# Kernel tuning notes

Hardware: AMD Instinct MI355X
Metric: run time of the kernel (lower is better)

The kernel has to match this reference:

```python
import jax, jax.numpy as jnp
import numpy as np

CONFIDENCE = 0.1
EPS = 1e-3  # keras BatchNormalization default epsilon
B, H, W, C = 4, 64, 64, 256


def setup_inputs() -> dict:
    key = jax.random.key(0)
    ks = jax.random.split(key, 6)
    return {
        "x": jax.random.normal(ks[0], (B, H, W, C), jnp.float32),
        "ca_gamma": jnp.ones((C,), jnp.float32),
        "ca_beta": jnp.zeros((C,), jnp.float32),
        "ca_mean": jnp.zeros((C,), jnp.float32),
        "ca_var": jnp.ones((C,), jnp.float32),
        "wq": jax.random.normal(ks[1], (C, C), jnp.float32) * 0.05,
        "wk": jax.random.normal(ks[2], (C, C), jnp.float32) * 0.05,
        "wv": jax.random.normal(ks[3], (C, C), jnp.float32) * 0.05,
        "wp": jax.random.normal(ks[4], (C, C), jnp.float32) * 0.05,
        "bn_gamma": jnp.ones((C,), jnp.float32),
        "bn_beta": jnp.zeros((C,), jnp.float32),
        "bn_mean": jnp.zeros((C,), jnp.float32),
        "bn_var": jnp.ones((C,), jnp.float32),
        "w_qkv": jax.random.normal(ks[5], (C, 3), jnp.float32) * 0.05,
    }


def _bn(x, g, b, m, v):
    # keras BatchNormalization, inference mode
    return (x - m) * jax.lax.rsqrt(v + EPS) * g + b


def reference(x, ca_gamma, ca_beta, ca_mean, ca_var, wq, wk, wv, wp,
              bn_gamma, bn_beta, bn_mean, bn_var, w_qkv):
    b, h, w, c = x.shape
    # ---- ChannelAttention (TRACER Channel_Tracer; dropout = identity at inference) ----
    gap = x.mean(axis=(1, 2))                         # [B, C] global average pool
    gn = _bn(gap, ca_gamma, ca_beta, ca_mean, ca_var)  # [B, C]
    q = gn @ wq                                        # 1x1 conv on 1x1 map == matmul
    k = gn @ wk
    v = gn @ wv
    logits = q[:, :, None] * k[:, None, :]             # [B, C, C], head_dim = 1
    score = jax.nn.softmax(logits, axis=-1)
    att = jnp.einsum('bij,bj->bi', score, v)           # [B, C]
    cmask = jax.nn.sigmoid(att @ wp)                   # [B, C] channel mask (alpha)
    ca_out = x * cmask[:, None, None, :] + x           # residual channel re-weighting
    # ---- UnionAttention spatial part ----
    co = _bn(ca_out, bn_gamma, bn_beta, bn_mean, bn_var)
    thr = jnp.percentile(cmask, CONFIDENCE * 100.0, axis=-1,
                         keepdims=True, method='linear')  # [B, 1]
    pmask = jnp.where(cmask > thr, cmask, 0.0)          # percentile masking
    co = co * pmask[:, None, None, :]
    qkv = jnp.einsum('bhwc,cf->bhwf', co, w_qkv)        # [B, H, W, 3] fused q/k/v 1x1 conv
    n = h * w
    qs = qkv[..., 0].reshape(b, n)                      # [B, N], head_dim = 1
    ks_ = qkv[..., 1].reshape(b, n)
    vs = qkv[..., 2].reshape(b, n)
    sl = qs[:, :, None] * ks_[:, None, :]               # [B, N, N] scores (outer product)
    sw = jax.nn.softmax(sl, axis=-1)
    sa = jnp.einsum('bij,bj->bi', sw, vs)               # [B, N]
    return qkv[..., 2:3] + sa.reshape(b, h, w, 1)       # v + attention, [B, H, W, 1]
```

## Files before the change

kernel.cpp:

```cpp
#include <hip/hip_runtime.h>

#define EPS 1e-3f

#define OFF_PGAP   0
#define OFF_PART   65536
#define OFF_AW     163840
#define OFF_BIAS   164864
#define OFF_QS     164880
#define OFF_KS     181264
#define OFF_VS     197648

__global__ __launch_bounds__(512) void k_gap(
    const float* __restrict__ x,
    const float* __restrict__ wq, const float* __restrict__ wk,
    const float* __restrict__ wv, const float* __restrict__ wp,
    const float* __restrict__ bng, const float* __restrict__ bnb,
    const float* __restrict__ bnm, const float* __restrict__ bnv,
    const float* __restrict__ cag, const float* __restrict__ cab,
    const float* __restrict__ cam, const float* __restrict__ cav,
    float* __restrict__ pgap)
{
    __shared__ float4 s4[512];
    int blk = blockIdx.x;
    int t = threadIdx.x;
    int lane = t & 63, sub = t >> 6;

    if (t < 256) {
        const float* wmat = (blk < 64) ? wq : (blk < 128) ? wk
                          : (blk < 192) ? wv : wp;
        float4 w4 = *(const float4*)(wmat + (size_t)(blk & 63) * 1024 + 4 * t);
        asm volatile("" :: "v"(w4.x), "v"(w4.y), "v"(w4.z), "v"(w4.w));
    }
    if (blk == 1 && t < 256) {
        float z = bng[t] + bnb[t] + bnm[t] + bnv[t];
        asm volatile("" :: "v"(z));
    }
    if (blk == 2 && t < 256) {
        float z = cag[t] + cab[t] + cam[t] + cav[t];
        asm volatile("" :: "v"(z));
    }

    const float* xp = x + ((size_t)blk * 64 + sub * 8) * 256 + 4 * lane;
    float4 s = make_float4(0.f, 0.f, 0.f, 0.f);
    #pragma unroll
    for (int u = 0; u < 8; ++u) {
        float4 v = *(const float4*)(xp + (size_t)u * 256);
        s.x += v.x; s.y += v.y; s.z += v.z; s.w += v.w;
    }
    s4[sub * 64 + lane] = s;
    __syncthreads();
    if (t < 64) {
        float4 o = s4[t];
        #pragma unroll
        for (int p = 1; p < 8; ++p) {
            float4 v = s4[p * 64 + t];
            o.x += v.x; o.y += v.y; o.z += v.z; o.w += v.w;
        }
        *(float4*)(pgap + blk * 256 + 4 * t) = o;
    }
}

__global__ __launch_bounds__(512) void k_qkvmat(
    const float* __restrict__ pgap,
    const float* __restrict__ cag, const float* __restrict__ cab,
    const float* __restrict__ cam, const float* __restrict__ cav,
    const float* __restrict__ wq, const float* __restrict__ wk,
    const float* __restrict__ wv,
    float* __restrict__ part)
{
    __shared__ float gpart[512];
    __shared__ float gn_s[32];
    __shared__ float red[2048];
    int blk = blockIdx.x;
    int m = blk / 32, g = blk % 32;
    int r0 = g * 8;
    int t = threadIdx.x;
    const float* W = (m == 0) ? wq : (m == 1) ? wk : wv;

    {
        int b = t >> 7, row = (t >> 4) & 7, p4 = t & 15;
        float s = 0.f;
        #pragma unroll
        for (int q = 0; q < 4; ++q)
            s += pgap[(size_t)(b * 64 + p4 * 4 + q) * 256 + r0 + row];
        gpart[b * 128 + row * 16 + p4] = s;
    }
    __syncthreads();
    if (t < 32) {
        int b = t >> 3, row = t & 7;
        float s = 0.f;
        #pragma unroll
        for (int p = 0; p < 16; ++p) s += gpart[b * 128 + row * 16 + p];
        float gv = s * (1.0f / 4096.0f);
        int c = r0 + row;
        float sc = cag[c] * rsqrtf(cav[c] + EPS);
        gn_s[b * 8 + row] = gv * sc + (cab[c] - cam[c] * sc);
    }
    __syncthreads();
    {
        int c = t & 255, h = t >> 8;
        float a0 = 0.f, a1 = 0.f, a2 = 0.f, a3 = 0.f;
        #pragma unroll
        for (int rr = 0; rr < 4; ++rr) {
            int ri = h * 4 + rr;
            float w = W[(size_t)(r0 + ri) * 256 + c];
            a0 = fmaf(gn_s[0 * 8 + ri], w, a0);
            a1 = fmaf(gn_s[1 * 8 + ri], w, a1);
            a2 = fmaf(gn_s[2 * 8 + ri], w, a2);
            a3 = fmaf(gn_s[3 * 8 + ri], w, a3);
        }
        red[(h * 4 + 0) * 256 + c] = a0;
        red[(h * 4 + 1) * 256 + c] = a1;
        red[(h * 4 + 2) * 256 + c] = a2;
        red[(h * 4 + 3) * 256 + c] = a3;
    }
    __syncthreads();
    {
        int b = t >> 7, c0 = (t & 127) * 2;
        float v0 = red[b * 256 + c0]     + red[(4 + b) * 256 + c0];
        float v1 = red[b * 256 + c0 + 1] + red[(4 + b) * 256 + c0 + 1];
        *(float2*)(part + (size_t)((m * 32 + g) * 4 + b) * 256 + c0) =
            make_float2(v0, v1);
    }
}

__global__ __launch_bounds__(512) void k_mid(
    const float* __restrict__ part, const float* __restrict__ wp,
    const float* __restrict__ bng, const float* __restrict__ bnb,
    const float* __restrict__ bnm, const float* __restrict__ bnv,
    const float* __restrict__ wqkv,
    float* __restrict__ Aw, float* __restrict__ biasW)
{
    __shared__ float sq[256], sk[256], sv[256], att[256], cmv[256], Bc[256];
    __shared__ float red[2048];
    __shared__ float swq[768];
    __shared__ float sc2[8];
    int b = blockIdx.x;
    int t = threadIdx.x;
    int lane = t & 63, sub = t >> 6;

    if (t < 384) { swq[t] = wqkv[t]; swq[t + 384] = wqkv[t + 384]; }

    if (t < 384) {
        int m = t >> 7, c0 = (t & 127) * 2;
        float a0 = 0.f, a1 = 0.f;
        #pragma unroll 8
        for (int g = 0; g < 32; ++g) {
            float2 v = *(const float2*)(part +
                          (size_t)((m * 32 + g) * 4 + b) * 256 + c0);
            a0 += v.x; a1 += v.y;
        }
        float* dst = (m == 0) ? sq : (m == 1) ? sk : sv;
        dst[c0] = a0; dst[c0 + 1] = a1;
    }
    __syncthreads();

    if (t < 64) {
        float mx = -1e30f, mn = 1e30f;
        #pragma unroll
        for (int u = 0; u < 4; ++u) {
            float v = sk[t + u * 64];
            mx = fmaxf(mx, v); mn = fminf(mn, v);
        }
        #pragma unroll
        for (int m2 = 1; m2 < 64; m2 <<= 1) {
            mx = fmaxf(mx, __shfl_xor(mx, m2, 64));
            mn = fminf(mn, __shfl_xor(mn, m2, 64));
        }
        if (t == 0) { sc2[0] = mx; sc2[1] = mn; }
    }
    __syncthreads();

    {
        int c = t & 255, h = t >> 8;
        float a = sq[c];
        float m = (a >= 0.f) ? a * sc2[0] : a * sc2[1];
        const float* skp = sk + h * 128;
        const float* svp = sv + h * 128;
        float den = 0.f, num = 0.f;
        #pragma unroll 4
        for (int j = 0; j < 128; ++j) {
            float e = __expf(fmaf(a, skp[j], -m));
            den += e; num = fmaf(e, svp[j], num);
        }
        red[h * 256 + c] = den;
        red[512 + h * 256 + c] = num;
    }
    __syncthreads();
    if (t < 256)
        att[t] = (red[512 + t] + red[768 + t]) / (red[t] + red[256 + t]);
    __syncthreads();

    {
        int rg = sub, c4 = lane * 4;
        float4 ac = make_float4(0.f, 0.f, 0.f, 0.f);
        const float* wpp = wp + (size_t)rg * 32 * 256 + c4;
        #pragma unroll 8
        for (int i = 0; i < 32; ++i) {
            float g = att[rg * 32 + i];
            float4 w = *(const float4*)(wpp + (size_t)i * 256);
            ac.x = fmaf(g, w.x, ac.x); ac.y = fmaf(g, w.y, ac.y);
            ac.z = fmaf(g, w.z, ac.z); ac.w = fmaf(g, w.w, ac.w);
        }
        *(float4*)(red + rg * 256 + c4) = ac;
    }
    __syncthreads();
    if (t < 256) {
        float ac = 0.f;
        #pragma unroll
        for (int r = 0; r < 8; ++r) ac += red[r * 256 + t];
        cmv[t] = 1.0f / (1.0f + __expf(-ac));
    }
    __syncthreads();

    if (t < 256) {
        float my = cmv[t];
        int rank = 0;
        for (int j = 0; j < 256; ++j) {
            float o = cmv[j];
            rank += (o < my) ? 1 : ((o == my && j < t) ? 1 : 0);
        }
        if (rank == 25) sc2[2] = my;
        if (rank == 26) sc2[3] = my;
    }
    __syncthreads();
    if (t == 0) sc2[4] = sc2[2] + 0.5f * (sc2[3] - sc2[2]);
    __syncthreads();

    if (t < 256) {
        float s2 = bng[t] * rsqrtf(bnv[t] + EPS);
        float o2 = bnb[t] - bnm[t] * s2;
        float cc = cmv[t];
        float pm = (cc > sc2[4]) ? cc : 0.f;
        Aw[b * 256 + t] = (1.f + cc) * s2 * pm;
        Bc[t] = o2 * pm;
    }
    __syncthreads();
    if (t < 3) {
        float s3 = 0.f;
        for (int ch = 0; ch < 256; ++ch)
            s3 = fmaf(Bc[ch], swq[ch * 3 + t], s3);
        biasW[b * 3 + t] = s3;
    }
}

__global__ __launch_bounds__(256) void k_qkv(
    const float* __restrict__ x, const float* __restrict__ A,
    const float* __restrict__ wqkv, const float* __restrict__ bias,
    float* __restrict__ qs, float* __restrict__ ks, float* __restrict__ vs)
{
    int lane = threadIdx.x & 63;
    int wid = (blockIdx.x * 256 + threadIdx.x) >> 6;
    float4 wA = *(const float4*)(wqkv + 12 * lane);
    float4 wB = *(const float4*)(wqkv + 12 * lane + 4);
    float4 wC = *(const float4*)(wqkv + 12 * lane + 8);
    float w00 = wA.x, w01 = wA.y, w02 = wA.z;
    float w10 = wA.w, w11 = wB.x, w12 = wB.y;
    float w20 = wB.z, w21 = wB.w, w22 = wC.x;
    float w30 = wC.y, w31 = wC.z, w32 = wC.w;
    #pragma unroll
    for (int b = 0; b < 4; ++b) {
        int pix = b * 4096 + wid;
        float4 xv = *(const float4*)(x + (size_t)pix * 256 + 4 * lane);
        float4 A4 = *(const float4*)(A + b * 256 + 4 * lane);
        float t0 = xv.x * A4.x, t1 = xv.y * A4.y;
        float t2 = xv.z * A4.z, t3 = xv.w * A4.w;
        float q = t0 * w00 + t1 * w10 + t2 * w20 + t3 * w30;
        float k = t0 * w01 + t1 * w11 + t2 * w21 + t3 * w31;
        float v = t0 * w02 + t1 * w12 + t2 * w22 + t3 * w32;
        #pragma unroll
        for (int m = 1; m < 64; m <<= 1) {
            q += __shfl_xor(q, m, 64);
            k += __shfl_xor(k, m, 64);
            v += __shfl_xor(v, m, 64);
        }
        if (lane == 0) {
            qs[pix] = q + bias[b * 3 + 0];
            ks[pix] = k + bias[b * 3 + 1];
            vs[pix] = v + bias[b * 3 + 2];
        }
    }
}

__global__ __launch_bounds__(512) void k_attn2(
    const float* __restrict__ qs, const float* __restrict__ ks,
    const float* __restrict__ vs, float* __restrict__ out)
{
    __shared__ float4 skv[2048];
    __shared__ float pden[8][64], pnum[8][64];
    __shared__ float rmax[8], rmin[8];
    int blk = blockIdx.x;
    int b = blk >> 6, ic = blk & 63;
    int t = threadIdx.x;
    int lane = t & 63, sub = t >> 6;
    int base = b * 4096;

    const float4* k4 = (const float4*)(ks + base);
    const float4* v4 = (const float4*)(vs + base);
    float kmx = -1e30f, kmn = 1e30f;
    #pragma unroll
    for (int u = 0; u < 2; ++u) {
        int i = t + u * 512;
        float4 kk = k4[i], vv = v4[i];
        skv[i * 2]     = make_float4(kk.x, vv.x, kk.y, vv.y);
        skv[i * 2 + 1] = make_float4(kk.z, vv.z, kk.w, vv.w);
        kmx = fmaxf(kmx, fmaxf(fmaxf(kk.x, kk.y), fmaxf(kk.z, kk.w)));
        kmn = fminf(kmn, fminf(fminf(kk.x, kk.y), fminf(kk.z, kk.w)));
    }
    #pragma unroll
    for (int m2 = 1; m2 < 64; m2 <<= 1) {
        kmx = fmaxf(kmx, __shfl_xor(kmx, m2, 64));
        kmn = fminf(kmn, __shfl_xor(kmn, m2, 64));
    }
    if (lane == 0) { rmax[sub] = kmx; rmin[sub] = kmn; }
    __syncthreads();
    float mx = rmax[0], mn = rmin[0];
    #pragma unroll
    for (int s = 1; s < 8; ++s) { mx = fmaxf(mx, rmax[s]); mn = fminf(mn, rmin[s]); }

    int row = ic * 64 + lane;
    float a = qs[base + row];
    float m = (a >= 0.f) ? a * mx : a * mn;
    float den0 = 0.f, num0 = 0.f, den1 = 0.f, num1 = 0.f;
    const float4* sp = skv + sub * 256;
    #pragma unroll 4
    for (int j = 0; j < 256; ++j) {
        float4 kv = sp[j];
        float e0 = __expf(fmaf(a, kv.x, -m));
        float e1 = __expf(fmaf(a, kv.z, -m));
        den0 += e0; num0 = fmaf(e0, kv.y, num0);
        den1 += e1; num1 = fmaf(e1, kv.w, num1);
    }
    pden[sub][lane] = den0 + den1;
    pnum[sub][lane] = num0 + num1;
    __syncthreads();
    if (t < 64) {
        float den = 0.f, num = 0.f;
        #pragma unroll
        for (int s = 0; s < 8; ++s) { den += pden[s][t]; num += pnum[s][t]; }
        int r = ic * 64 + t;
        float vrow = (r & 1) ? skv[r >> 1].w : skv[r >> 1].y;
        out[base + r] = vrow + num / den;
    }
}

extern "C" void kernel_launch(void* const* d_in, const int* in_sizes, int n_in,
                              void* d_out, int out_size, void* d_ws, size_t ws_size,
                              hipStream_t stream) {
    const float* x    = (const float*)d_in[0];
    const float* cag  = (const float*)d_in[1];
    const float* cab  = (const float*)d_in[2];
    const float* cam  = (const float*)d_in[3];
    const float* cav  = (const float*)d_in[4];
    const float* wq   = (const float*)d_in[5];
    const float* wk   = (const float*)d_in[6];
    const float* wv   = (const float*)d_in[7];
    const float* wp   = (const float*)d_in[8];
    const float* bng  = (const float*)d_in[9];
    const float* bnb  = (const float*)d_in[10];
    const float* bnm  = (const float*)d_in[11];
    const float* bnv  = (const float*)d_in[12];
    const float* wqkv = (const float*)d_in[13];

    float* ws   = (float*)d_ws;
    float* pgap = ws + OFF_PGAP;
    float* part = ws + OFF_PART;
    float* Aw   = ws + OFF_AW;
    float* bias = ws + OFF_BIAS;
    float* qs   = ws + OFF_QS;
    float* ks   = ws + OFF_KS;
    float* vs   = ws + OFF_VS;

    k_gap<<<dim3(256), dim3(512), 0, stream>>>(x, wq, wk, wv, wp,
                                               bng, bnb, bnm, bnv,
                                               cag, cab, cam, cav, pgap);
    k_qkvmat<<<dim3(96), dim3(512), 0, stream>>>(pgap, cag, cab, cam, cav,
                                                 wq, wk, wv, part);
    k_mid<<<dim3(4), dim3(512), 0, stream>>>(part, wp, bng, bnb, bnm, bnv,
                                             wqkv, Aw, bias);
    k_qkv<<<dim3(1024), dim3(256), 0, stream>>>(x, Aw, wqkv, bias, qs, ks, vs);
    k_attn2<<<dim3(256), dim3(512), 0, stream>>>(qs, ks, vs, (float*)d_out);
}
```

Before: 130.5 us.

## Fuse qkv matmul and mid stage via last-block atomic counter; widen qkv projection

Merges k_qkvmat and k_mid into one kernel: every block writes its partial products with agent-scope stores, increments a global counter, and the last four blocks of each generation wait on the counter and then run the per-batch softmax, percentile and mask stage. This removes one kernel launch and the gap between launches. k_qkv now has each wave handle two pixels with 8 channels per lane, halving the grid and the shuffle depth. Both softmax loops switch to exp2 with log2(e) pre-scaling. The spin-wait relies on all 96 blocks being co-resident and on a persistent modulo-96 counter, which carries deadlock and ordering risk.

```diff
diff --git a/kernel.cpp b/kernel.cpp
--- a/kernel.cpp
+++ b/kernel.cpp
@@ -3,12 +3,22 @@
 #define EPS 1e-3f
 
 #define OFF_PGAP   0
-#define OFF_PART   65536
-#define OFF_AW     163840
-#define OFF_BIAS   164864
-#define OFF_QS     164880
-#define OFF_KS     181264
-#define OFF_VS     197648
+#define OFF_PART   81920
+#define OFF_AW     196608
+#define OFF_BIAS   198656
+#define OFF_QS     215040
+#define OFF_KS     231424
+#define OFF_VS     247808
+
+#define L2E 1.4426950408889634f
+
+__device__ __forceinline__ void st_wt2(float* p, float a, float b) {
+    union { float f[2]; unsigned long long u; } x; x.f[0] = a; x.f[1] = b;
+    __hip_atomic_store((unsigned long long*)p, x.u, __ATOMIC_RELAXED,
+                       __HIP_MEMORY_SCOPE_AGENT);
+}
+
+__device__ unsigned g_done;
 
 __global__ __launch_bounds__(512) void k_gap(
     const float* __restrict__ x,
@@ -60,187 +70,211 @@
     }
 }
 
-__global__ __launch_bounds__(512) void k_qkvmat(
+__global__ __launch_bounds__(512) void k_qkvmid(
     const float* __restrict__ pgap,
     const float* __restrict__ cag, const float* __restrict__ cab,
     const float* __restrict__ cam, const float* __restrict__ cav,
     const float* __restrict__ wq, const float* __restrict__ wk,
-    const float* __restrict__ wv,
-    float* __restrict__ part)
+    const float* __restrict__ wv, const float* __restrict__ wp,
+    const float* __restrict__ bng, const float* __restrict__ bnb,
+    const float* __restrict__ bnm, const float* __restrict__ bnv,
+    const float* __restrict__ wqkv,
+    float* __restrict__ part, float* __restrict__ Aw, float* __restrict__ biasW)
 {
-    __shared__ float gpart[512];
-    __shared__ float gn_s[32];
-    __shared__ float red[2048];
+    __shared__ float smem[4360];
+    __shared__ int sBatch;
     int blk = blockIdx.x;
     int m = blk / 32, g = blk % 32;
     int r0 = g * 8;
     int t = threadIdx.x;
+    int lane = t & 63, sub = t >> 6;
     const float* W = (m == 0) ? wq : (m == 1) ? wk : wv;
 
     {
-        int b = t >> 7, row = (t >> 4) & 7, p4 = t & 15;
-        float s = 0.f;
-        #pragma unroll
-        for (int q = 0; q < 4; ++q)
-            s += pgap[(size_t)(b * 64 + p4 * 4 + q) * 256 + r0 + row];
-        gpart[b * 128 + row * 16 + p4] = s;
+        float* gpart = smem;
+        float* gn_s  = smem + 512;
+        float* red   = smem + 1536;
+        {
+            int b = t >> 7, row = (t >> 4) & 7, p4 = t & 15;
+            float s = 0.f;
+            #pragma unroll
+            for (int q = 0; q < 4; ++q)
+                s += pgap[(size_t)(b * 64 + p4 * 4 + q) * 256 + r0 + row];
+            gpart[b * 128 + row * 16 + p4] = s;
+        }
+        __syncthreads();
+        if (t < 32) {
+            int b = t >> 3, row = t & 7;
+            float s = 0.f;
+            #pragma unroll
+            for (int p = 0; p < 16; ++p) s += gpart[b * 128 + row * 16 + p];
+            float gv = s * (1.0f / 4096.0f);
+            int c = r0 + row;
+            float sc = cag[c] * rsqrtf(cav[c] + EPS);
+            gn_s[b * 8 + row] = gv * sc + (cab[c] - cam[c] * sc);
+        }
+        __syncthreads();
+        {
+            int c = t & 255, h = t >> 8;
+            float a0 = 0.f, a1 = 0.f, a2 = 0.f, a3 = 0.f;
+            #pragma unroll
+            for (int rr = 0; rr < 4; ++rr) {
+                int ri = h * 4 + rr;
+                float w = W[(size_t)(r0 + ri) * 256 + c];
+                a0 = fmaf(gn_s[0 * 8 + ri], w, a0);
+                a1 = fmaf(gn_s[1 * 8 + ri], w, a1);
+                a2 = fmaf(gn_s[2 * 8 + ri], w, a2);
+                a3 = fmaf(gn_s[3 * 8 + ri], w, a3);
+            }
+            red[(h * 4 + 0) * 256 + c] = a0;
+            red[(h * 4 + 1) * 256 + c] = a1;
+            red[(h * 4 + 2) * 256 + c] = a2;
+            red[(h * 4 + 3) * 256 + c] = a3;
+        }
+        __syncthreads();
+        {
+            int b = t >> 7, c0 = (t & 127) * 2;
+            float v0 = red[b * 256 + c0]     + red[(4 + b) * 256 + c0];
+            float v1 = red[b * 256 + c0 + 1] + red[(4 + b) * 256 + c0 + 1];
+            st_wt2(part + (size_t)((m * 32 + g) * 4 + b) * 256 + c0, v0, v1);
+        }
     }
     __syncthreads();
-    if (t < 32) {
-        int b = t >> 3, row = t & 7;
-        float s = 0.f;
-        #pragma unroll
-        for (int p = 0; p < 16; ++p) s += gpart[b * 128 + row * 16 + p];
-        float gv = s * (1.0f / 4096.0f);
-        int c = r0 + row;
-        float sc = cag[c] * rsqrtf(cav[c] + EPS);
-        gn_s[b * 8 + row] = gv * sc + (cab[c] - cam[c] * sc);
+    if (t == 0) {
+        unsigned v = __hip_atomic_fetch_add(&g_done, 1u, __ATOMIC_ACQ_REL,
+                                            __HIP_MEMORY_SCOPE_AGENT);
+        unsigned r = v % 96u;
+        int batch = (int)r - 92;
+        if (batch >= 0) {
+            unsigned target = v - r + 96u;
+            unsigned tries = 0;
+            while (__hip_atomic_load(&g_done, __ATOMIC_RELAXED,
+                                     __HIP_MEMORY_SCOPE_AGENT) < target) {
+                __builtin_amdgcn_s_sleep(1);
+                if (++tries > 8000000u) break;
+            }
+        }
+        sBatch = batch;
     }
     __syncthreads();
+    if (sBatch < 0) return;
+
     {
-        int c = t & 255, h = t >> 8;
-        float a0 = 0.f, a1 = 0.f, a2 = 0.f, a3 = 0.f;
-        #pragma unroll
-        for (int rr = 0; rr < 4; ++rr) {
-            int ri = h * 4 + rr;
-            float w = W[(size_t)(r0 + ri) * 256 + c];
-            a0 = fmaf(gn_s[0 * 8 + ri], w, a0);
-            a1 = fmaf(gn_s[1 * 8 + ri], w, a1);
-            a2 = fmaf(gn_s[2 * 8 + ri], w, a2);
-            a3 = fmaf(gn_s[3 * 8 + ri], w, a3);
-        }
-        red[(h * 4 + 0) * 256 + c] = a0;
-        red[(h * 4 + 1) * 256 + c] = a1;
-        red[(h * 4 + 2) * 256 + c] = a2;
-        red[(h * 4 + 3) * 256 + c] = a3;
-    }
-    __syncthreads();
-    {
-        int b = t >> 7, c0 = (t & 127) * 2;
-        float v0 = red[b * 256 + c0]     + red[(4 + b) * 256 + c0];
-        float v1 = red[b * 256 + c0 + 1] + red[(4 + b) * 256 + c0 + 1];
-        *(float2*)(part + (size_t)((m * 32 + g) * 4 + b) * 256 + c0) =
-            make_float2(v0, v1);
-    }
-}
-
-__global__ __launch_bounds__(512) void k_mid(
-    const float* __restrict__ part, const float* __restrict__ wp,
-    const float* __restrict__ bng, const float* __restrict__ bnb,
-    const float* __restrict__ bnm, const float* __restrict__ bnv,
-    const float* __restrict__ wqkv,
-    float* __restrict__ Aw, float* __restrict__ biasW)
-{
-    __shared__ float sq[256], sk[256], sv[256], att[256], cmv[256], Bc[256];
-    __shared__ float red[2048];
-    __shared__ float swq[768];
-    __shared__ float sc2[8];
-    int b = blockIdx.x;
-    int t = threadIdx.x;
-    int lane = t & 63, sub = t >> 6;
-
-    if (t < 384) { swq[t] = wqkv[t]; swq[t + 384] = wqkv[t + 384]; }
-
-    if (t < 384) {
-        int m = t >> 7, c0 = (t & 127) * 2;
-        float a0 = 0.f, a1 = 0.f;
-        #pragma unroll 8
-        for (int g = 0; g < 32; ++g) {
-            float2 v = *(const float2*)(part +
-                          (size_t)((m * 32 + g) * 4 + b) * 256 + c0);
-            a0 += v.x; a1 += v.y;
-        }
-        float* dst = (m == 0) ? sq : (m == 1) ? sk : sv;
-        dst[c0] = a0; dst[c0 + 1] = a1;
-    }
-    __syncthreads();
-
-    if (t < 64) {
-        float mx = -1e30f, mn = 1e30f;
-        #pragma unroll
-        for (int u = 0; u < 4; ++u) {
-            float v = sk[t + u * 64];
-            mx = fmaxf(mx, v); mn = fminf(mn, v);
-        }
-        #pragma unroll
-        for (int m2 = 1; m2 < 64; m2 <<= 1) {
-            mx = fmaxf(mx, __shfl_xor(mx, m2, 64));
-            mn = fminf(mn, __shfl_xor(mn, m2, 64));
-        }
-        if (t == 0) { sc2[0] = mx; sc2[1] = mn; }
-    }
-    __syncthreads();
-
-    {
-        int c = t & 255, h = t >> 8;
-        float a = sq[c];
-        float m = (a >= 0.f) ? a * sc2[0] : a * sc2[1];
-        const float* skp = sk + h * 128;
-        const float* svp = sv + h * 128;
-        float den = 0.f, num = 0.f;
-        #pragma unroll 4
-        for (int j = 0; j < 128; ++j) {
-            float e = __expf(fmaf(a, skp[j], -m));
-            den += e; num = fmaf(e, svp[j], num);
-        }
-        red[h * 256 + c] = den;
-        red[512 + h * 256 + c] = num;
-    }
-    __syncthreads();
-    if (t < 256)
-        att[t] = (red[512 + t] + red[768 + t]) / (red[t] + red[256 + t]);
-    __syncthreads();
-
-    {
-        int rg = sub, c4 = lane * 4;
-        float4 ac = make_float4(0.f, 0.f, 0.f, 0.f);
-        const float* wpp = wp + (size_t)rg * 32 * 256 + c4;
-        #pragma unroll 8
-        for (int i = 0; i < 32; ++i) {
-            float g = att[rg * 32 + i];
-            float4 w = *(const float4*)(wpp + (size_t)i * 256);
-            ac.x = fmaf(g, w.x, ac.x); ac.y = fmaf(g, w.y, ac.y);
-            ac.z = fmaf(g, w.z, ac.z); ac.w = fmaf(g, w.w, ac.w);
-        }
-        *(float4*)(red + rg * 256 + c4) = ac;
-    }
-    __syncthreads();
-    if (t < 256) {
-        float ac = 0.f;
-        #pragma unroll
-        for (int r = 0; r < 8; ++r) ac += red[r * 256 + t];
-        cmv[t] = 1.0f / (1.0f + __expf(-ac));
-    }
-    __syncthreads();
-
-    if (t < 256) {
-        float my = cmv[t];
-        int rank = 0;
-        for (int j = 0; j < 256; ++j) {
-            float o = cmv[j];
-            rank += (o < my) ? 1 : ((o == my && j < t) ? 1 : 0);
-        }
-        if (rank == 25) sc2[2] = my;
-        if (rank == 26) sc2[3] = my;
-    }
-    __syncthreads();
-    if (t == 0) sc2[4] = sc2[2] + 0.5f * (sc2[3] - sc2[2]);
-    __syncthreads();
-
-    if (t < 256) {
-        float s2 = bng[t] * rsqrtf(bnv[t] + EPS);
-        float o2 = bnb[t] - bnm[t] * s2;
-        float cc = cmv[t];
-        float pm = (cc > sc2[4]) ? cc : 0.f;
-        Aw[b * 256 + t] = (1.f + cc) * s2 * pm;
-        Bc[t] = o2 * pm;
-    }
-    __syncthreads();
-    if (t < 3) {
-        float s3 = 0.f;
-        for (int ch = 0; ch < 256; ++ch)
-            s3 = fmaf(Bc[ch], swq[ch * 3 + t], s3);
-        biasW[b * 3 + t] = s3;
+        int b = sBatch;
+        float* sq  = smem;
+        float* sk  = smem + 256;
+        float* sv  = smem + 512;
+        float* att = smem + 768;
+        float* cmv = smem + 1024;
+        float* Bc  = smem + 1280;
+        float* red = smem + 1536;
+        float* swq = smem + 3584;
+        float* sc2 = smem + 4352;
+
+        if (t < 384) { swq[t] = wqkv[t]; swq[t + 384] = wqkv[t + 384]; }
+
+        if (t < 384) {
+            int mm = t >> 7, c0 = (t & 127) * 2;
+            float a0 = 0.f, a1 = 0.f;
+            #pragma unroll 8
+            for (int gg = 0; gg < 32; ++gg) {
+                float2 v = *(const float2*)(part +
+                              (size_t)((mm * 32 + gg) * 4 + b) * 256 + c0);
+                a0 += v.x; a1 += v.y;
+            }
+            float* dst = (mm == 0) ? sq : (mm == 1) ? sk : sv;
+            dst[c0] = a0; dst[c0 + 1] = a1;
+        }
+        __syncthreads();
+
+        if (t < 64) {
+            float mx = -1e30f, mn = 1e30f;
+            #pragma unroll
+            for (int u = 0; u < 4; ++u) {
+                float v = sk[t + u * 64];
+                mx = fmaxf(mx, v); mn = fminf(mn, v);
+            }
+            #pragma unroll
+            for (int m2 = 1; m2 < 64; m2 <<= 1) {
+                mx = fmaxf(mx, __shfl_xor(mx, m2, 64));
+                mn = fminf(mn, __shfl_xor(mn, m2, 64));
+            }
+            if (t == 0) { sc2[0] = mx; sc2[1] = mn; }
+        }
+        __syncthreads();
+
+        {
+            int c = t & 255, h = t >> 8;
+            float a = sq[c];
+            float mrow = (a >= 0.f) ? a * sc2[0] : a * sc2[1];
+            float a2 = a * L2E, m2 = mrow * L2E;
+            const float* skp = sk + h * 128;
+            const float* svp = sv + h * 128;
+            float den = 0.f, num = 0.f;
+            #pragma unroll 4
+            for (int j = 0; j < 128; ++j) {
+                float e = __builtin_amdgcn_exp2f(fmaf(a2, skp[j], -m2));
+                den += e; num = fmaf(e, svp[j], num);
+            }
+            red[h * 256 + c] = den;
+            red[512 + h * 256 + c] = num;
+        }
+        __syncthreads();
+        if (t < 256)
+            att[t] = (red[512 + t] + red[768 + t]) / (red[t] + red[256 + t]);
+        __syncthreads();
+
+        {
+            int rg = sub, c4 = lane * 4;
+            float4 ac = make_float4(0.f, 0.f, 0.f, 0.f);
+            const float* wpp = wp + (size_t)rg * 32 * 256 + c4;
+            #pragma unroll 8
+            for (int i = 0; i < 32; ++i) {
+                float gv = att[rg * 32 + i];
+                float4 w = *(const float4*)(wpp + (size_t)i * 256);
+                ac.x = fmaf(gv, w.x, ac.x); ac.y = fmaf(gv, w.y, ac.y);
+                ac.z = fmaf(gv, w.z, ac.z); ac.w = fmaf(gv, w.w, ac.w);
+            }
+            *(float4*)(red + rg * 256 + c4) = ac;
+        }
+        __syncthreads();
+        if (t < 256) {
+            float ac = 0.f;
+            #pragma unroll
+            for (int r = 0; r < 8; ++r) ac += red[r * 256 + t];
+            cmv[t] = 1.0f / (1.0f + __expf(-ac));
+        }
+        __syncthreads();
+
+        if (t < 256) {
+            float my = cmv[t];
+            int rank = 0;
+            for (int j = 0; j < 256; ++j) {
+                float o = cmv[j];
+                rank += (o < my) ? 1 : ((o == my && j < t) ? 1 : 0);
+            }
+            if (rank == 25) sc2[2] = my;
+            if (rank == 26) sc2[3] = my;
+        }
+        __syncthreads();
+        if (t == 0) sc2[4] = sc2[2] + 0.5f * (sc2[3] - sc2[2]);
+        __syncthreads();
+
+        if (t < 256) {
+            float s2 = bng[t] * rsqrtf(bnv[t] + EPS);
+            float o2 = bnb[t] - bnm[t] * s2;
+            float cc = cmv[t];
+            float pm = (cc > sc2[4]) ? cc : 0.f;
+            Aw[b * 256 + t] = (1.f + cc) * s2 * pm;
+            Bc[t] = o2 * pm;
+        }
+        __syncthreads();
+        if (t < 3) {
+            float s3 = 0.f;
+            for (int ch = 0; ch < 256; ++ch)
+                s3 = fmaf(Bc[ch], swq[ch * 3 + t], s3);
+            biasW[b * 3 + t] = s3;
+        }
     }
 }
 
@@ -249,35 +283,44 @@
     const float* __restrict__ wqkv, const float* __restrict__ bias,
     float* __restrict__ qs, float* __restrict__ ks, float* __restrict__ vs)
 {
-    int lane = threadIdx.x & 63;
-    int wid = (blockIdx.x * 256 + threadIdx.x) >> 6;
-    float4 wA = *(const float4*)(wqkv + 12 * lane);
-    float4 wB = *(const float4*)(wqkv + 12 * lane + 4);
-    float4 wC = *(const float4*)(wqkv + 12 * lane + 8);
-    float w00 = wA.x, w01 = wA.y, w02 = wA.z;
-    float w10 = wA.w, w11 = wB.x, w12 = wB.y;
-    float w20 = wB.z, w21 = wB.w, w22 = wC.x;
-    float w30 = wC.y, w31 = wC.z, w32 = wC.w;
+    int t = threadIdx.x;
+    int lane = t & 63;
+    int sl = lane & 31;
+    int half = lane >> 5;
+    int wid = (blockIdx.x * 256 + t) >> 6;
+    union { float4 v4[6]; float f[24]; } W;
+    #pragma unroll
+    for (int i = 0; i < 6; ++i)
+        W.v4[i] = *(const float4*)(wqkv + 24 * sl + 4 * i);
     #pragma unroll
     for (int b = 0; b < 4; ++b) {
-        int pix = b * 4096 + wid;
-        float4 xv = *(const float4*)(x + (size_t)pix * 256 + 4 * lane);
-        float4 A4 = *(const float4*)(A + b * 256 + 4 * lane);
-        float t0 = xv.x * A4.x, t1 = xv.y * A4.y;
-        float t2 = xv.z * A4.z, t3 = xv.w * A4.w;
-        float q = t0 * w00 + t1 * w10 + t2 * w20 + t3 * w30;
-        float k = t0 * w01 + t1 * w11 + t2 * w21 + t3 * w31;
-        float v = t0 * w02 + t1 * w12 + t2 * w22 + t3 * w32;
+        int pix = b * 4096 + wid * 2 + half;
+        const float* xp = x + (size_t)pix * 256 + sl * 8;
+        float4 xv0 = *(const float4*)(xp);
+        float4 xv1 = *(const float4*)(xp + 4);
+        float4 a0 = *(const float4*)(A + b * 256 + sl * 8);
+        float4 a1 = *(const float4*)(A + b * 256 + sl * 8 + 4);
+        float bq = bias[b * 3 + 0];
+        float bk = bias[b * 3 + 1];
+        float bv = bias[b * 3 + 2];
+        float tt0 = xv0.x * a0.x, tt1 = xv0.y * a0.y;
+        float tt2 = xv0.z * a0.z, tt3 = xv0.w * a0.w;
+        float tt4 = xv1.x * a1.x, tt5 = xv1.y * a1.y;
+        float tt6 = xv1.z * a1.z, tt7 = xv1.w * a1.w;
+        float q = tt0 * W.f[0] + tt1 * W.f[3] + tt2 * W.f[6] + tt3 * W.f[9]
+                + tt4 * W.f[12] + tt5 * W.f[15] + tt6 * W.f[18] + tt7 * W.f[21];
+        float k = tt0 * W.f[1] + tt1 * W.f[4] + tt2 * W.f[7] + tt3 * W.f[10]
+                + tt4 * W.f[13] + tt5 * W.f[16] + tt6 * W.f[19] + tt7 * W.f[22];
+        float v = tt0 * W.f[2] + tt1 * W.f[5] + tt2 * W.f[8] + tt3 * W.f[11]
+                + tt4 * W.f[14] + tt5 * W.f[17] + tt6 * W.f[20] + tt7 * W.f[23];
         #pragma unroll
-        for (int m = 1; m < 64; m <<= 1) {
-            q += __shfl_xor(q, m, 64);
-            k += __shfl_xor(k, m, 64);
-            v += __shfl_xor(v, m, 64);
-        }
-        if (lane == 0) {
-            qs[pix] = q + bias[b * 3 + 0];
-            ks[pix] = k + bias[b * 3 + 1];
-            vs[pix] = v + bias[b * 3 + 2];
+        for (int m2 = 1; m2 < 32; m2 <<= 1) {
+            q += __shfl_xor(q, m2, 64);
+            k += __shfl_xor(k, m2, 64);
+            v += __shfl_xor(v, m2, 64);
+        }
+        if (sl == 0) {
+            qs[pix] = q + bq; ks[pix] = k + bk; vs[pix] = v + bv;
         }
     }
 }
@@ -320,14 +363,15 @@
 
     int row = ic * 64 + lane;
     float a = qs[base + row];
-    float m = (a >= 0.f) ? a * mx : a * mn;
+    float mrow = (a >= 0.f) ? a * mx : a * mn;
+    float a2 = a * L2E, m2v = mrow * L2E;
     float den0 = 0.f, num0 = 0.f, den1 = 0.f, num1 = 0.f;
     const float4* sp = skv + sub * 256;
     #pragma unroll 4
     for (int j = 0; j < 256; ++j) {
         float4 kv = sp[j];
-        float e0 = __expf(fmaf(a, kv.x, -m));
-        float e1 = __expf(fmaf(a, kv.z, -m));
+        float e0 = __builtin_amdgcn_exp2f(fmaf(a2, kv.x, -m2v));
+        float e1 = __builtin_amdgcn_exp2f(fmaf(a2, kv.z, -m2v));
         den0 += e0; num0 = fmaf(e0, kv.y, num0);
         den1 += e1; num1 = fmaf(e1, kv.w, num1);
     }
@@ -374,10 +418,10 @@
     k_gap<<<dim3(256), dim3(512), 0, stream>>>(x, wq, wk, wv, wp,
                                                bng, bnb, bnm, bnv,
                                                cag, cab, cam, cav, pgap);
-    k_qkvmat<<<dim3(96), dim3(512), 0, stream>>>(pgap, cag, cab, cam, cav,
-                                                 wq, wk, wv, part);
-    k_mid<<<dim3(4), dim3(512), 0, stream>>>(part, wp, bng, bnb, bnm, bnv,
-                                             wqkv, Aw, bias);
-    k_qkv<<<dim3(1024), dim3(256), 0, stream>>>(x, Aw, wqkv, bias, qs, ks, vs);
+    k_qkvmid<<<dim3(96), dim3(512), 0, stream>>>(pgap, cag, cab, cam, cav,
+                                                 wq, wk, wv, wp,
+                                                 bng, bnb, bnm, bnv, wqkv,
+                                                 part, Aw, bias);
+    k_qkv<<<dim3(512), dim3(256), 0, stream>>>(x, Aw, wqkv, bias, qs, ks, vs);
     k_attn2<<<dim3(256), dim3(512), 0, stream>>>(qs, ks, vs, (float*)d_out);
 }
```

Result: faster. 126.8 us, median of 2 (-2.8%).
